# Optimization experiments

Hardware: AMD Instinct MI355X
Metric: run time of the kernel (lower is better)

The kernel has to match this reference:

```python
import jax, jax.numpy as jnp
import numpy as np

KSIZE, SCALE, STRIDE, SOFTMAX_SCALE = 3, 3, 1, 10.0
ESCAPE_NAN = 1e-4
DN = ('NCHW', 'OIHW', 'NCHW')


def same_pad(x, k, stride):
    # torch same_padding: pad so out = ceil(in/stride)
    H, W = x.shape[-2], x.shape[-1]
    oh, ow = -(-H // stride), -(-W // stride)
    ph = max(0, (oh - 1) * stride + k - H)
    pw = max(0, (ow - 1) * stride + k - W)
    return jnp.pad(x, ((0, 0), (0, 0), (ph // 2, ph - ph // 2), (pw // 2, pw - pw // 2)))


def extract_patches(img, k, stride):
    # img [B,C,H,W] already padded -> [B, L, C, k, k], matching torch Unfold ordering (C slowest, kh, kw)
    B, C, H, W = img.shape
    oh, ow = (H - k) // stride + 1, (W - k) // stride + 1
    cols = [img[:, :, i:i + stride * oh:stride, j:j + stride * ow:stride]
            for i in range(k) for j in range(k)]
    p = jnp.stack(cols, axis=2)                      # [B, C, k*k, oh, ow]
    p = p.reshape(B, C, k, k, oh * ow)               # [B, C, k, k, L]
    return jnp.transpose(p, (0, 4, 1, 2, 3))         # [B, L, C, k, k]


def conv1x1_prelu(x, W, b, a):
    y = jnp.einsum('bchw,oc->bohw', x, W) + b[None, :, None, None]
    return jnp.where(y >= 0, y, a * y)


def bilinear_down(x, Ho, Wo):
    # F.interpolate(mode='bilinear', align_corners=False), no antialias
    H, W = x.shape[-2], x.shape[-1]
    def coords(o, s):
        src = (jnp.arange(o, dtype=jnp.float32) + 0.5) * (s / o) - 0.5
        src = jnp.clip(src, 0.0, s - 1.0)
        i0 = jnp.floor(src).astype(jnp.int32)
        i1 = jnp.minimum(i0 + 1, s - 1)
        return i0, i1, src - i0.astype(jnp.float32)
    y0, y1, wy = coords(Ho, H)
    x0, x1, wx = coords(Wo, W)
    r = x[:, :, y0, :] * (1.0 - wy)[:, None] + x[:, :, y1, :] * wy[:, None]
    return r[:, :, :, x0] * (1.0 - wx) + r[:, :, :, x1] * wx


def forward(x, Wa, ba, aa, Wm1, bm1, am1, Wm2, bm2, am2):
    B, C, H, W = x.shape
    kernel = SCALE * KSIZE  # 9
    embed_w = conv1x1_prelu(x, Wa, ba, aa)      # [B,C,H,W]
    match = conv1x1_prelu(x, Wm1, bm1, am1)     # [B,C/2,H,W]
    # large-scale patches used as conv_transpose kernels: [B, L, C, 9, 9]
    raw_w = extract_patches(same_pad(embed_w, kernel, STRIDE * SCALE), kernel, STRIDE * SCALE)
    Hr, Wr = H // SCALE, W // SCALE
    ref = conv1x1_prelu(bilinear_down(x, Hr, Wr), Wm2, bm2, am2)  # [B,C/2,Hr,Wr]
    # small-scale patches used as correlation kernels: [B, L, C/2, 3, 3]
    w = extract_patches(same_pad(ref, KSIZE, STRIDE), KSIZE, STRIDE)
    norm = jnp.sqrt(jnp.sum(w * w, axis=(2, 3, 4), keepdims=True))
    wn = w / jnp.maximum(norm, ESCAPE_NAN)
    xp = same_pad(match, KSIZE, 1)  # [B,C/2,H+2,W+2]

    def corr(xi, wi):  # xi [C/2,H+2,W+2], wi [L,C/2,3,3] -> [L,H,W]
        return jax.lax.conv_general_dilated(xi[None], wi, (1, 1), 'VALID', dimension_numbers=DN)[0]

    y = jax.vmap(corr)(xp, wn)                  # [B,L,H,W]
    y = jax.nn.softmax(y * SOFTMAX_SCALE, axis=1)

    pad = kernel - 1 - SCALE  # conv_transpose2d(stride=3, padding=3) equivalent padding = 5

    def tconv(yi, rwi):  # yi [L,H,W], rwi [L,C,9,9] -> [C,3H,3W]
        k = jnp.transpose(jnp.flip(rwi, (-2, -1)), (1, 0, 2, 3))  # [C,L,9,9]
        return jax.lax.conv_general_dilated(
            yi[None], k, (1, 1), [(pad, pad), (pad, pad)],
            lhs_dilation=(STRIDE * SCALE, STRIDE * SCALE), dimension_numbers=DN)[0]

    out = jax.vmap(tconv)(y, raw_w) / 6.0       # [B,C,3H,3W]
    return out


def setup_inputs() -> dict:
    key = jax.random.key(0)
    ks = jax.random.split(key, 8)
    B, C, H, W = 4, 64, 60, 60
    C2 = C // 2
    return {
        'x': jax.random.normal(ks[0], (B, C, H, W), jnp.float32),
        'Wa': jax.random.normal(ks[1], (C, C), jnp.float32) * 0.1,
        'ba': jax.random.normal(ks[2], (C,), jnp.float32) * 0.1,
        'aa': jnp.full((1,), 0.25, jnp.float32),
        'Wm1': jax.random.normal(ks[3], (C2, C), jnp.float32) * 0.1,
        'bm1': jax.random.normal(ks[4], (C2,), jnp.float32) * 0.1,
        'am1': jnp.full((1,), 0.25, jnp.float32),
        'Wm2': jax.random.normal(ks[5], (C2, C), jnp.float32) * 0.1,
        'bm2': jax.random.normal(ks[6], (C2,), jnp.float32) * 0.1,
        'am2': jnp.full((1,), 0.25, jnp.float32),
    }


def reference(x, Wa, ba, aa, Wm1, bm1, am1, Wm2, bm2, am2):
    return forward(x, Wa, ba, aa, Wm1, bm1, am1, Wm2, bm2, am2)
```

## Files before the change

kernel.cpp:

```cpp
#include <hip/hip_runtime.h>
#include <hip/hip_bf16.h>

typedef __hip_bfloat16 bf16_t;
using f32x4  = __attribute__((ext_vector_type(4))) float;
using bf16x8 = __attribute__((ext_vector_type(8))) short;

#define NB 4
#define NC 64
#define NC2 32
#define NH 60
#define NW 60
#define NPIX (NH*NW)
#define HP 66
#define MP 62
#define HR 20
#define RP 22
#define NL 400
#define OHW 180
#define KPAD 512

#define OFF_XPB   2230272
#define OFF_REFP  3214336
#define OFF_YBL   3462144
#define OFF_AP    14982144
#define OFF_EB    29727744
#define OFF_XP    32087040
#define OFF_RF    40381440

__global__ __launch_bounds__(256) void k_conv(
    const float* __restrict__ x,
    const float* __restrict__ Wa,  const float* __restrict__ ba,  const float* __restrict__ aa,
    const float* __restrict__ Wm1, const float* __restrict__ bm1, const float* __restrict__ am1,
    const float* __restrict__ Wm2, const float* __restrict__ bm2, const float* __restrict__ am2,
    bf16_t* __restrict__ E_bt, bf16_t* __restrict__ xpb, float* __restrict__ refp) {
  int bid = blockIdx.x;
  int t = threadIdx.x;
  if (bid < 300) {
    __shared__ float Ws[64*64];
    __shared__ float bs[64];
    __shared__ float al;
    int b = bid / 75, pblk = bid % 75;
    for (int i = t; i < 64*64; i += 256) {
      int co = i >> 6, c = i & 63;
      Ws[c*64 + co] = Wa[i];
    }
    if (t < 64) bs[t] = ba[t];
    if (t == 0) al = aa[0];
    __syncthreads();
    int lane = t & 63, wid = t >> 6;
    int pix0 = pblk*48 + wid*12;
    const float* xb = x + b*NC*NPIX + pix0;
    float acc[12];
    #pragma unroll
    for (int p = 0; p < 12; ++p) acc[p] = bs[lane];
    for (int c = 0; c < 64; ++c) {
      float wv = Ws[c*64 + lane];
      const float* xc = xb + c*NPIX;
      #pragma unroll
      for (int p = 0; p < 12; ++p)
        acc[p] = fmaf(xc[p], wv, acc[p]);
    }
    #pragma unroll
    for (int p = 0; p < 12; ++p) {
      float v = acc[p];
      v = v >= 0.f ? v : al*v;
      int pix = pix0 + p;
      int ph = pix / NW, pw = pix % NW;
      E_bt[((b*HP + ph+3)*HP + (pw+3))*NC + lane] = __float2bfloat16(v);
    }
  } else if (bid < 2100) {
    int idx = (bid - 300)*256 + t;
    int pix = idx % NPIX; int tmp = idx / NPIX;
    int co = tmp % NC2; int b = tmp / NC2;
    float alpha = am1[0];
    const float* xb = x + b*NC*NPIX + pix;
    const float* wr = Wm1 + co*64;
    float acc = bm1[co];
    #pragma unroll 8
    for (int c = 0; c < 64; ++c)
      acc = fmaf(xb[c*NPIX], wr[c], acc);
    acc = acc >= 0.f ? acc : alpha*acc;
    int ph = pix / NW, pw = pix % NW;
    xpb[((b*NC2 + co)*MP + ph+1)*MP + (pw+1)] = __float2bfloat16(acc);
  } else if (bid < 2300) {
    int idx = (bid - 2100)*256 + t;
    int pos = idx % (HR*HR); int tmp = idx / (HR*HR);
    int co = tmp % NC2; int b = tmp / NC2;
    int hr = pos / HR, wr_ = pos % HR;
    float alpha = am2[0];
    const float* xb = x + b*NC*NPIX + (3*hr+1)*NW + (3*wr_+1);
    const float* wrow = Wm2 + co*64;
    float acc = bm2[co];
    #pragma unroll 8
    for (int c = 0; c < 64; ++c)
      acc = fmaf(xb[c*NPIX], wrow[c], acc);
    acc = acc >= 0.f ? acc : alpha*acc;
    refp[((b*NC2 + co)*RP + hr+1)*RP + (wr_+1)] = acc;
  } else {
    unsigned short* Eu = (unsigned short*)E_bt;
    unsigned short* Xu = (unsigned short*)xpb;
    int g0 = (bid - 2300)*256 + t;
    for (int g = g0; g < 235520; g += 80*256) {
      if (g < 193536) {
        int b = g / 48384, e = g % 48384;
        int addr;
        if (e < 25344) {
          int r6 = e / 4224, off = e % 4224;
          int ph = (r6 < 3) ? r6 : 60 + r6;
          addr = (b*HP + ph)*4224 + off;
        } else {
          int e2 = e - 25344;
          int row = e2 / 384, off2 = e2 % 384;
          int pos = (off2 < 192) ? off2 : 4032 + (off2 - 192);
          addr = (b*HP + 3 + row)*4224 + pos;
        }
        Eu[addr] = 0;
      } else if (g < 224768) {
        int gg = g - 193536;
        int p = gg / 244, e = gg % 244;
        int pos;
        if (e < 62) pos = e;
        else if (e < 124) pos = 3782 + (e - 62);
        else { int i = e - 124; pos = (1 + (i >> 1))*62 + (i & 1)*61; }
        Xu[p*3844 + pos] = 0;
      } else {
        int gg = g - 224768;
        int p = gg / 84, e = gg % 84;
        int pos;
        if (e < 22) pos = e;
        else if (e < 44) pos = 462 + (e - 22);
        else { int i = e - 44; pos = (1 + (i >> 1))*22 + (i & 1)*21; }
        refp[p*484 + pos] = 0.f;
      }
    }
  }
}

__global__ __launch_bounds__(256) void k_swz(
    const bf16_t* __restrict__ xpb, const float* __restrict__ refp,
    const bf16_t* __restrict__ E_bt,
    bf16_t* __restrict__ Xp, bf16_t* __restrict__ Rf, bf16_t* __restrict__ Eb) {
  __shared__ float scl[16];
  int bid = blockIdx.x;
  int t = threadIdx.x;
  if (bid < 2025) {
    int tid = bid*256 + t;
    int slot = tid & 63; int rest = tid >> 6;
    int ks = rest % 9; int rest2 = rest / 9;
    int mblk = rest2 % 225; int b = rest2 / 225;
    int m = mblk*16 + (slot & 15);
    int h = m / NW, w = m % NW;
    int k0 = ks*32 + (slot >> 4)*8;
    const bf16_t* xb = xpb + (size_t)b*NC2*MP*MP;
    union { bf16_t a[8]; bf16x8 v; } u;
    #pragma unroll
    for (int j = 0; j < 8; ++j) {
      int k = k0 + j;
      int c = k / 9, r = k % 9;
      int i = r / 3, j2 = r % 3;
      u.a[j] = xb[(c*MP + h + i)*MP + w + j2];
    }
    *(bf16x8*)(Xp + (size_t)tid*8) = u.v;
  } else if (bid < 2125) {
    int r2 = bid - 2025;
    int nblk = r2 % 25, b = r2 / 25;
    int ll = t >> 4, sub = t & 15;
    int l = nblk*16 + ll;
    int lh = l / HR, lw = l % HR;
    const float* rb = refp + (size_t)b*NC2*RP*RP;
    float ss = 0.f;
    #pragma unroll
    for (int e0 = 0; e0 < 18; ++e0) {
      int e = sub*18 + e0;
      int c = e / 9, r = e % 9;
      int i = r / 3, j = r % 3;
      float v = rb[(c*RP + lh + i)*RP + lw + j];
      ss = fmaf(v, v, ss);
    }
    #pragma unroll
    for (int off = 1; off < 16; off <<= 1)
      ss += __shfl_xor(ss, off);
    if (sub == 0) scl[ll] = 10.f / fmaxf(sqrtf(ss), 1e-4f);
    __syncthreads();
    for (int sidx = t; sidx < 576; sidx += 256) {
      int ks = sidx >> 6, slot = sidx & 63;
      int l2 = nblk*16 + (slot & 15);
      int lh2 = l2 / HR, lw2 = l2 % HR;
      float sc = scl[slot & 15];
      int k0 = ks*32 + (slot >> 4)*8;
      union { bf16_t a[8]; bf16x8 v; } u;
      #pragma unroll
      for (int j = 0; j < 8; ++j) {
        int k = k0 + j;
        int c = k / 9, r = k % 9;
        int i = r / 3, j2 = r % 3;
        u.a[j] = __float2bfloat16(rb[(c*RP + lh2 + i)*RP + lw2 + j2] * sc);
      }
      *(bf16x8*)(Rf + ((size_t)(b*25 + nblk)*576 + sidx)*8) = u.v;
    }
  } else {
    int r2 = bid - 2125;
    int n = r2 % 576, b = r2 / 576;
    int c = n / 9, n9 = n % 9, rr = n9 / 3, s = n9 % 3;
    size_t nbase = ((size_t)(b*12 + n/48)*16);
    const unsigned short* Eu = (const unsigned short*)E_bt;
    unsigned short* Ebu = (unsigned short*)Eb;
    for (int k = t; k < KPAD; k += 256) {
      unsigned short v = 0;
      if (k < 484) {
        int u = k / 22, vv = k % 22;
        v = Eu[((size_t)((b*HP + 3*u + rr)*HP + 3*vv + s))*NC + c];
      }
      size_t idx = (((nbase + (k>>5))*3 + (n%48)/16)*64 + ((k>>3)&3)*16 + (n&15))*8 + (k&7);
      Ebu[idx] = v;
    }
  }
}

__global__ __launch_bounds__(64) void k_cgemm(
    const bf16x8* __restrict__ Xp, const bf16x8* __restrict__ Rf,
    bf16_t* __restrict__ y_bl) {
  __shared__ __align__(16) bf16_t ytile[48][80];
  int L = threadIdx.x;
  int o = blockIdx.x;
  int xcd = o & 7, sl = o >> 3;
  int w = (xcd < 4 ? xcd*188 : 752 + (xcd-4)*187) + sl;
  int b = w / 375; int rem = w % 375;
  int mt = rem / 5, nt = rem % 5;
  const bf16x8* pa = Xp + ((size_t)(b*225 + mt*3)*9)*64 + L;
  const bf16x8* pb = Rf + ((size_t)(b*25 + nt*5)*9)*64 + L;
  f32x4 acc[3][5];
  #pragma unroll
  for (int i = 0; i < 3; ++i)
    #pragma unroll
    for (int j = 0; j < 5; ++j)
      acc[i][j] = {0.f, 0.f, 0.f, 0.f};
  bf16x8 A[3][3], B[3][5];
  #pragma unroll
  for (int i = 0; i < 3; ++i) { A[0][i] = pa[i*576]; A[1][i] = pa[i*576 + 64]; }
  #pragma unroll
  for (int j = 0; j < 5; ++j) { B[0][j] = pb[j*576]; B[1][j] = pb[j*576 + 64]; }
  #pragma unroll
  for (int ks = 0; ks < 9; ++ks) {
    if (ks < 7) {
      #pragma unroll
      for (int i = 0; i < 3; ++i) A[(ks+2)%3][i] = pa[i*576 + (ks+2)*64];
      #pragma unroll
      for (int j = 0; j < 5; ++j) B[(ks+2)%3][j] = pb[j*576 + (ks+2)*64];
    }
    #pragma unroll
    for (int i = 0; i < 3; ++i)
      #pragma unroll
      for (int j = 0; j < 5; ++j)
        acc[i][j] = __builtin_amdgcn_mfma_f32_16x16x32_bf16(A[ks%3][i], B[ks%3][j], acc[i][j], 0, 0, 0);
  }
  int quad = L >> 4, col = L & 15;
  #pragma unroll
  for (int mf = 0; mf < 3; ++mf)
    #pragma unroll
    for (int r = 0; r < 4; ++r)
      #pragma unroll
      for (int nf = 0; nf < 5; ++nf)
        ytile[mf*16 + quad*4 + r][nf*16 + col] = __float2bfloat16(acc[mf][nf][r]);
  __syncthreads();
  bf16_t* dst0 = y_bl + ((size_t)(b*NPIX + mt*48))*NL + nt*80;
  for (int i = L; i < 480; i += 64) {
    int row = i / 10, seg = i % 10;
    *(bf16x8*)(dst0 + (size_t)row*NL + seg*8) = *(const bf16x8*)&ytile[row][seg*8];
  }
}

__device__ __forceinline__ float lo_bf(unsigned int u) {
  return __uint_as_float(u << 16);
}
__device__ __forceinline__ float hi_bf(unsigned int u) {
  return __uint_as_float(u & 0xffff0000u);
}
__device__ __forceinline__ float u16_bf(unsigned short u) {
  return __uint_as_float(((unsigned int)u) << 16);
}
__device__ __forceinline__ unsigned short bf_bits(float f) {
  union { bf16_t h; unsigned short u; } c;
  c.h = __float2bfloat16(f);
  return c.u;
}

__global__ __launch_bounds__(512) void k_saprime(
    const unsigned int* __restrict__ y_b32, bf16_t* __restrict__ Ap) {
  __shared__ uint4 raw[2592];
  unsigned short* ysp = (unsigned short*)raw;
  int t = threadIdx.x;
  int b = blockIdx.z;
  int h0base = blockIdx.y*4, w0base = blockIdx.x*4;
  for (int i = t; i < 2592; i += 512) raw[i] = uint4{0,0,0,0};
  __syncthreads();

  int wave = t >> 6, lane = t & 63;
  bool act = lane < 50;
  for (int pos = wave; pos < 36; pos += 8) {
    int i = pos / 6, jj = pos % 6;
    int hh = h0base - 1 + i, ww = w0base - 1 + jj;
    if (!((unsigned)hh < NH && (unsigned)ww < NW)) continue;
    const uint4* src4 = (const uint4*)(y_b32 + ((size_t)(b*NPIX + hh*NW + ww))*200);
    uint4 v = act ? src4[lane] : uint4{0,0,0,0};
    float f[8];
    if (act) {
      f[0] = lo_bf(v.x); f[1] = hi_bf(v.x);
      f[2] = lo_bf(v.y); f[3] = hi_bf(v.y);
      f[4] = lo_bf(v.z); f[5] = hi_bf(v.z);
      f[6] = lo_bf(v.w); f[7] = hi_bf(v.w);
    } else {
      #pragma unroll
      for (int k = 0; k < 8; ++k) f[k] = -1e30f;
    }
    float m = -1e30f;
    #pragma unroll
    for (int k = 0; k < 8; ++k) m = fmaxf(m, f[k]);
    #pragma unroll
    for (int off = 32; off > 0; off >>= 1)
      m = fmaxf(m, __shfl_xor(m, off));
    float s = 0.f;
    #pragma unroll
    for (int k = 0; k < 8; ++k) {
      float e = __expf(f[k] - m);
      f[k] = e;
      s += e;
    }
    #pragma unroll
    for (int off = 32; off > 0; off >>= 1)
      s += __shfl_xor(s, off);
    float r = 1.f / s;
    if (act) {
      #pragma unroll
      for (int k = 0; k < 4; ++k) {
        int l2 = lane*4 + k;
        int lh = l2 / 10, lw = 2*l2 - 20*lh;
        union { bf16_t h[2]; unsigned int u; } pk;
        pk.h[0] = __float2bfloat16(f[2*k]   * r);
        pk.h[1] = __float2bfloat16(f[2*k+1] * r);
        *(unsigned int*)&ysp[pos*576 + (lh+2)*24 + (lw+2)] = pk.u;
      }
    }
  }
  __syncthreads();

  int row = t >> 5;
  int klane = t & 31;
  int h0r = row >> 2, w0r = row & 3;
  int m = (h0base + h0r)*NW + (w0base + w0r);
  int pblk = m / 80, pf = (m % 80) >> 4, mrow = m & 15;
  size_t rowbase = ((size_t)(b*45 + pblk)*16);
  const unsigned short* basep = ysp + (h0r*6 + w0r)*576;
  unsigned short* Apu = (unsigned short*)Ap;
  for (int kk = 0; kk < 8; ++kk) {
    int k = kk*64 + 2*klane;
    float a0 = 0.f, a1 = 0.f;
    if (k < 484) {
      int u = k / 22, v = k - 22*u;
      const unsigned short* q = basep + u*24 + v;
      #pragma unroll
      for (int dh = 0; dh < 3; ++dh) {
        unsigned int p0 = *(const unsigned int*)(q + dh*3480);
        a0 += lo_bf(p0); a1 += hi_bf(p0);
        a0 += u16_bf(q[dh*3480 + 577]);
        a1 += u16_bf(q[dh*3480 + 578]);
        unsigned int p2 = *(const unsigned int*)(q + dh*3480 + 1154);
        a0 += lo_bf(p2); a1 += hi_bf(p2);
      }
    }
    unsigned int pk = ((unsigned int)bf_bits(a1) << 16) | bf_bits(a0);
    size_t idx = (((rowbase + (k>>5))*5 + pf)*64 + ((k>>3)&3)*16 + mrow)*8 + (k&7);
    *(unsigned int*)&Apu[idx] = pk;
  }
}

__global__ __launch_bounds__(64) void k_tgemm(
    const bf16x8* __restrict__ Eb, const bf16x8* __restrict__ Ap,
    float* __restrict__ out) {
  __shared__ __align__(16) float otile[80][52];
  int L = threadIdx.x;
  int o = blockIdx.x;
  int w = (o & 7)*270 + (o >> 3);
  int b = w / 540; int rem = w % 540;
  int pbi = rem / 12, rb = rem % 12;
  const bf16x8* pa = Eb + ((size_t)(b*12 + rb)*16)*3*64 + L;
  const bf16x8* pp = Ap + ((size_t)(b*45 + pbi)*16)*5*64 + L;
  f32x4 acc[3][5];
  #pragma unroll
  for (int i = 0; i < 3; ++i)
    #pragma unroll
    for (int j = 0; j < 5; ++j)
      acc[i][j] = {0.f, 0.f, 0.f, 0.f};
  bf16x8 A[3][3], B[3][5];
  #pragma unroll
  for (int i = 0; i < 3; ++i) { A[0][i] = pa[i*64]; A[1][i] = pa[192 + i*64]; }
  #pragma unroll
  for (int j = 0; j < 5; ++j) { B[0][j] = pp[j*64]; B[1][j] = pp[320 + j*64]; }
  #pragma unroll
  for (int ks = 0; ks < 16; ++ks) {
    if (ks < 14) {
      const bf16x8* na = pa + (ks+2)*192;
      const bf16x8* nb = pp + (ks+2)*320;
      #pragma unroll
      for (int i = 0; i < 3; ++i) A[(ks+2)%3][i] = na[i*64];
      #pragma unroll
      for (int j = 0; j < 5; ++j) B[(ks+2)%3][j] = nb[j*64];
    }
    #pragma unroll
    for (int i = 0; i < 3; ++i)
      #pragma unroll
      for (int j = 0; j < 5; ++j)
        acc[i][j] = __builtin_amdgcn_mfma_f32_16x16x32_bf16(A[ks%3][i], B[ks%3][j], acc[i][j], 0, 0, 0);
  }
  int quad = L >> 4, col = L & 15;
  const float sc = 1.f/6.f;
  #pragma unroll
  for (int pf = 0; pf < 5; ++pf)
    #pragma unroll
    for (int rf = 0; rf < 3; ++rf) {
      f32x4 v = acc[rf][pf];
      v[0] *= sc; v[1] *= sc; v[2] *= sc; v[3] *= sc;
      *(f32x4*)&otile[pf*16 + col][rf*16 + quad*4] = v;
    }
  __syncthreads();
  float* ob = out + b*(NC*OHW*OHW);
  int m0 = pbi*80;
  for (int i = L; i < 960; i += 64) {
    int p = i / 60, q = i % 60;
    int nl = rb*48 + p*3;
    int c = nl / 9, rr = (nl % 9) / 3;
    int f0 = q*4;
    f32x4 v;
    #pragma unroll
    for (int j = 0; j < 4; ++j) {
      int f = f0 + j;
      int mi = f / 3, s = f - 3*mi;
      v[j] = otile[mi][p*3 + s];
    }
    int mi0 = f0 / 3, s0 = f0 % 3;
    int m = m0 + mi0;
    int h0 = m / 60, w0 = m % 60;
    *(f32x4*)&ob[c*32400 + (3*h0 + rr)*180 + 3*w0 + s0] = v;
  }
}

extern "C" void kernel_launch(void* const* d_in, const int* in_sizes, int n_in,
                              void* d_out, int out_size, void* d_ws, size_t ws_size,
                              hipStream_t stream) {
  (void)in_sizes; (void)n_in; (void)out_size; (void)ws_size;
  const float* x   = (const float*)d_in[0];
  const float* Wa  = (const float*)d_in[1];
  const float* ba  = (const float*)d_in[2];
  const float* aa  = (const float*)d_in[3];
  const float* Wm1 = (const float*)d_in[4];
  const float* bm1 = (const float*)d_in[5];
  const float* am1 = (const float*)d_in[6];
  const float* Wm2 = (const float*)d_in[7];
  const float* bm2 = (const float*)d_in[8];
  const float* am2 = (const float*)d_in[9];
  float* out = (float*)d_out;

  char* base = (char*)d_ws;
  bf16_t* E_bt  = (bf16_t*)base;
  bf16_t* xpb   = (bf16_t*)(base + OFF_XPB);
  float*  refp  = (float*)(base + OFF_REFP);
  bf16_t* y_bl  = (bf16_t*)(base + OFF_YBL);
  bf16_t* ApSwz = (bf16_t*)(base + OFF_AP);
  bf16_t* EbSwz = (bf16_t*)(base + OFF_EB);
  bf16_t* XpSwz = (bf16_t*)(base + OFF_XP);
  bf16_t* RfSwz = (bf16_t*)(base + OFF_RF);

  k_conv<<<2380, 256, 0, stream>>>(x, Wa, ba, aa, Wm1, bm1, am1, Wm2, bm2, am2,
                                   E_bt, xpb, refp);
  k_swz<<<4429, 256, 0, stream>>>(xpb, refp, E_bt, XpSwz, RfSwz, EbSwz);
  k_cgemm<<<1500, 64, 0, stream>>>((const bf16x8*)XpSwz, (const bf16x8*)RfSwz, y_bl);
  k_saprime<<<dim3(15, 15, NB), 512, 0, stream>>>((const unsigned int*)y_bl, ApSwz);
  k_tgemm<<<2160, 64, 0, stream>>>((const bf16x8*)EbSwz, (const bf16x8*)ApSwz, out);
}
```

Before: 165.8 us.

## Share Ap tile across four waves via double-buffered LDS in k_tgemm

Reworks the final transposed-conv GEMM so each 256-thread block runs four waves over four row blocks that share one Ap (B operand) tile, staged through a double-buffered LDS buffer instead of each wave fetching it from global memory. The grid shrinks from 2160 to 540 blocks and the XCD-aware block remapping is updated to match. The epilogue now serialises the four waves through the single otile buffer with barriers. The cost is extra __syncthreads per k-step, the loss of the register prefetch pipeline for the A operand, and a serialised store phase.

```diff
diff --git a/kernel.cpp b/kernel.cpp
--- a/kernel.cpp
+++ b/kernel.cpp
@@ -374,73 +374,84 @@
   }
 }
 
-__global__ __launch_bounds__(64) void k_tgemm(
+__global__ __launch_bounds__(256) void k_tgemm(
     const bf16x8* __restrict__ Eb, const bf16x8* __restrict__ Ap,
     float* __restrict__ out) {
+  __shared__ __align__(16) bf16x8 apb[2][320];
   __shared__ __align__(16) float otile[80][52];
-  int L = threadIdx.x;
+  int t = threadIdx.x;
+  int L = t & 63, wid = t >> 6;
   int o = blockIdx.x;
-  int w = (o & 7)*270 + (o >> 3);
-  int b = w / 540; int rem = w % 540;
-  int pbi = rem / 12, rb = rem % 12;
+  int xcd = o & 7, sl = o >> 3;
+  int w = (xcd < 4 ? xcd*68 : 272 + (xcd-4)*67) + sl;
+  int b = w / 135; int rem = w % 135;
+  int pbi = rem / 3, rq = rem % 3;
+  int rb = rq*4 + wid;
   const bf16x8* pa = Eb + ((size_t)(b*12 + rb)*16)*3*64 + L;
-  const bf16x8* pp = Ap + ((size_t)(b*45 + pbi)*16)*5*64 + L;
+  const bf16x8* pp = Ap + ((size_t)(b*45 + pbi)*16)*5*64;
   f32x4 acc[3][5];
   #pragma unroll
   for (int i = 0; i < 3; ++i)
     #pragma unroll
     for (int j = 0; j < 5; ++j)
       acc[i][j] = {0.f, 0.f, 0.f, 0.f};
-  bf16x8 A[3][3], B[3][5];
-  #pragma unroll
-  for (int i = 0; i < 3; ++i) { A[0][i] = pa[i*64]; A[1][i] = pa[192 + i*64]; }
-  #pragma unroll
-  for (int j = 0; j < 5; ++j) { B[0][j] = pp[j*64]; B[1][j] = pp[320 + j*64]; }
-  #pragma unroll
+  for (int i = t; i < 320; i += 256) apb[0][i] = pp[i];
+  __syncthreads();
+  #pragma unroll 1
   for (int ks = 0; ks < 16; ++ks) {
-    if (ks < 14) {
-      const bf16x8* na = pa + (ks+2)*192;
-      const bf16x8* nb = pp + (ks+2)*320;
-      #pragma unroll
-      for (int i = 0; i < 3; ++i) A[(ks+2)%3][i] = na[i*64];
-      #pragma unroll
-      for (int j = 0; j < 5; ++j) B[(ks+2)%3][j] = nb[j*64];
-    }
+    if (ks < 15) {
+      const bf16x8* src = pp + (ks+1)*320;
+      for (int i = t; i < 320; i += 256) apb[(ks+1)&1][i] = src[i];
+    }
+    bf16x8 af[3], bf[5];
+    #pragma unroll
+    for (int i = 0; i < 3; ++i) af[i] = pa[ks*192 + i*64];
+    const bf16x8* abuf = apb[ks&1];
+    #pragma unroll
+    for (int j = 0; j < 5; ++j) bf[j] = abuf[j*64 + L];
     #pragma unroll
     for (int i = 0; i < 3; ++i)
       #pragma unroll
       for (int j = 0; j < 5; ++j)
-        acc[i][j] = __builtin_amdgcn_mfma_f32_16x16x32_bf16(A[ks%3][i], B[ks%3][j], acc[i][j], 0, 0, 0);
+        acc[i][j] = __builtin_amdgcn_mfma_f32_16x16x32_bf16(af[i], bf[j], acc[i][j], 0, 0, 0);
+    __syncthreads();
   }
   int quad = L >> 4, col = L & 15;
   const float sc = 1.f/6.f;
-  #pragma unroll
-  for (int pf = 0; pf < 5; ++pf)
-    #pragma unroll
-    for (int rf = 0; rf < 3; ++rf) {
-      f32x4 v = acc[rf][pf];
-      v[0] *= sc; v[1] *= sc; v[2] *= sc; v[3] *= sc;
-      *(f32x4*)&otile[pf*16 + col][rf*16 + quad*4] = v;
-    }
-  __syncthreads();
   float* ob = out + b*(NC*OHW*OHW);
   int m0 = pbi*80;
-  for (int i = L; i < 960; i += 64) {
-    int p = i / 60, q = i % 60;
-    int nl = rb*48 + p*3;
-    int c = nl / 9, rr = (nl % 9) / 3;
-    int f0 = q*4;
-    f32x4 v;
-    #pragma unroll
-    for (int j = 0; j < 4; ++j) {
-      int f = f0 + j;
-      int mi = f / 3, s = f - 3*mi;
-      v[j] = otile[mi][p*3 + s];
-    }
-    int mi0 = f0 / 3, s0 = f0 % 3;
-    int m = m0 + mi0;
-    int h0 = m / 60, w0 = m % 60;
-    *(f32x4*)&ob[c*32400 + (3*h0 + rr)*180 + 3*w0 + s0] = v;
+  #pragma unroll 1
+  for (int r = 0; r < 4; ++r) {
+    if (wid == r) {
+      #pragma unroll
+      for (int pf = 0; pf < 5; ++pf)
+        #pragma unroll
+        for (int rf = 0; rf < 3; ++rf) {
+          f32x4 v = acc[rf][pf];
+          v[0] *= sc; v[1] *= sc; v[2] *= sc; v[3] *= sc;
+          *(f32x4*)&otile[pf*16 + col][rf*16 + quad*4] = v;
+        }
+    }
+    __syncthreads();
+    int rbr = rq*4 + r;
+    for (int i = t; i < 960; i += 256) {
+      int p = i / 60, q = i % 60;
+      int nl = rbr*48 + p*3;
+      int c = nl / 9, rr = (nl % 9) / 3;
+      int f0 = q*4;
+      f32x4 v;
+      #pragma unroll
+      for (int j = 0; j < 4; ++j) {
+        int f = f0 + j;
+        int mi = f / 3, s = f - 3*mi;
+        v[j] = otile[mi][p*3 + s];
+      }
+      int mi0 = f0 / 3, s0 = f0 % 3;
+      int m = m0 + mi0;
+      int h0 = m / 60, w0 = m % 60;
+      *(f32x4*)&ob[c*32400 + (3*h0 + rr)*180 + 3*w0 + s0] = v;
+    }
+    __syncthreads();
   }
 }
 
@@ -475,5 +486,5 @@
   k_swz<<<4429, 256, 0, stream>>>(xpb, refp, E_bt, XpSwz, RfSwz, EbSwz);
   k_cgemm<<<1500, 64, 0, stream>>>((const bf16x8*)XpSwz, (const bf16x8*)RfSwz, y_bl);
   k_saprime<<<dim3(15, 15, NB), 512, 0, stream>>>((const unsigned int*)y_bl, ApSwz);
-  k_tgemm<<<2160, 64, 0, stream>>>((const bf16x8*)EbSwz, (const bf16x8*)ApSwz, out);
-}
+  k_tgemm<<<540, 256, 0, stream>>>((const bf16x8*)EbSwz, (const bf16x8*)ApSwz, out);
+}
```

Measured after the change: 173.2 us. 1.04x slower.
